# Kernel optimization log

Hardware: AMD Instinct MI355X
Metric: run time of the kernel (lower is better)

## Reference

```python
import jax, jax.numpy as jnp
import numpy as np

OWN_DIM = 7
INTR_DIM = 5
N_HEADS = 3
HEAD_DIM = 5
N_INTR = 256
ACT_DIM = 2
HID = 256
B = 16384


def setup_inputs() -> dict:
    key = jax.random.key(0)
    ks = jax.random.split(key, 16)
    def rn(k, shape, scale=0.1):
        return (jax.random.normal(k, shape, dtype=jnp.float32) * scale)
    obs = jax.random.normal(ks[0], (B, OWN_DIM + N_INTR * INTR_DIM), dtype=jnp.float32)
    in_dim = OWN_DIM + N_HEADS * HEAD_DIM  # 22
    return {
        "obs": obs,
        "Wq": rn(ks[1], (N_HEADS, HEAD_DIM, OWN_DIM)),
        "bq": rn(ks[2], (N_HEADS, HEAD_DIM)),
        "Wk": rn(ks[3], (N_HEADS, HEAD_DIM, INTR_DIM)),
        "bk": rn(ks[4], (N_HEADS, HEAD_DIM)),
        "Wv": rn(ks[5], (N_HEADS, HEAD_DIM, INTR_DIM)),
        "bv": rn(ks[6], (N_HEADS, HEAD_DIM)),
        "v_att": rn(ks[7], (N_HEADS, HEAD_DIM), 0.5),
        "temperature": jnp.ones((1,), dtype=jnp.float32) * 3.0,
        "W1": rn(ks[8], (in_dim, HID)),
        "b1": rn(ks[9], (HID,)),
        "W2": rn(ks[10], (HID, HID)),
        "b2": rn(ks[11], (HID,)),
        "Wf": rn(ks[12], (HID, ACT_DIM)),
        "bf": rn(ks[13], (ACT_DIM,)),
        "log_std": jnp.zeros((ACT_DIM,), dtype=jnp.float32),
    }


def reference(obs, Wq, bq, Wk, bk, Wv, bv, v_att, temperature,
              W1, b1, W2, b2, Wf, bf, log_std):
    own = obs[:, :OWN_DIM]                                   # [B,7]
    intr = obs[:, OWN_DIM:OWN_DIM + N_INTR * INTR_DIM].reshape(-1, N_INTR, INTR_DIM)  # [B,N,5]

    # per-head projections, all heads at once
    q = jnp.einsum('bo,hdo->bhd', own, Wq) + bq[None]        # [B,H,5]
    k = jnp.einsum('bni,hdi->bhnd', intr, Wk) + bk[None, :, None, :]  # [B,H,N,5]
    v = jnp.einsum('bni,hdi->bhnd', intr, Wv) + bv[None, :, None, :]  # [B,H,N,5]

    energy = jnp.tanh(q[:, :, None, :] + k)                  # [B,H,N,5]
    scores = jnp.einsum('bhnd,hd->bhn', energy, v_att)       # [B,H,N]
    scores = scores * jnp.abs(temperature)[0]

    is_padding = jnp.sum(jnp.abs(intr), axis=2) < 1e-6       # [B,N]
    scores = jnp.where(is_padding[:, None, :], -jnp.inf, scores)
    alpha = jax.nn.softmax(scores, axis=-1)                  # [B,H,N]
    alpha = jnp.nan_to_num(alpha, nan=0.0)

    context = jnp.einsum('bhn,bhnd->bhd', alpha, v).reshape(-1, N_HEADS * HEAD_DIM)  # [B,15]

    x = jnp.concatenate([own, context], axis=1)              # [B,22]
    x = jax.nn.leaky_relu(x @ W1 + b1, negative_slope=0.2)
    x = jax.nn.leaky_relu(x @ W2 + b2, negative_slope=0.2)
    out = x @ Wf + bf                                        # [B,2]
    log_std_exp = jnp.broadcast_to(log_std[None, :], (out.shape[0], ACT_DIM))
    return jnp.concatenate([out, log_std_exp], axis=1)       # [B,4]
```

## Files before the change

### kernel.cpp

```cpp
#include <hip/hip_runtime.h>
#include <math.h>

#define OWN_DIM 7
#define INTR_DIM 5
#define N_HEADS 3
#define HEAD_DIM 5
#define N_INTR 256
#define HID 256
#define BATCH 16384
#define ROW 1287

typedef __attribute__((ext_vector_type(8))) short bf16x8;
typedef __attribute__((ext_vector_type(4))) float f32x4;

__device__ __forceinline__ float fast_tanh(float x) {
    float e = __expf(2.0f * x);
    return 1.0f - 2.0f * __builtin_amdgcn_rcpf(e + 1.0f);
}

__device__ __forceinline__ float leaky(float x) {
    return x > 0.0f ? x : 0.2f * x;
}

__device__ __forceinline__ unsigned short f2bf(float f) {
    union { float f; unsigned u; } v; v.f = f;
    unsigned r = (v.u + 0x7FFFu + ((v.u >> 16) & 1u)) >> 16;
    return (unsigned short)r;
}

__device__ __forceinline__ unsigned pack2(unsigned short a, unsigned short b) {
    return (unsigned)a | ((unsigned)b << 16);
}

__global__ __launch_bounds__(256) void prep_kernel(
    const float* __restrict__ W1, const float* __restrict__ W2,
    unsigned short* __restrict__ W1t, unsigned short* __restrict__ W2t)
{
    int idx = blockIdx.x * 256 + threadIdx.x;
    int col = idx & 255;
    int kq = idx >> 8;
    ushort4 o;
    o.x = f2bf(W2[(kq * 4 + 0) * 256 + col]);
    o.y = f2bf(W2[(kq * 4 + 1) * 256 + col]);
    o.z = f2bf(W2[(kq * 4 + 2) * 256 + col]);
    o.w = f2bf(W2[(kq * 4 + 3) * 256 + col]);
    *((ushort4*)(W2t + col * 256 + kq * 4)) = o;
    if (kq < 8) {
        ushort4 p;
        int k = kq * 4;
        p.x = (k + 0) < 22 ? f2bf(W1[(k + 0) * 256 + col]) : 0;
        p.y = (k + 1) < 22 ? f2bf(W1[(k + 1) * 256 + col]) : 0;
        p.z = (k + 2) < 22 ? f2bf(W1[(k + 2) * 256 + col]) : 0;
        p.w = (k + 3) < 22 ? f2bf(W1[(k + 3) * 256 + col]) : 0;
        *((ushort4*)(W1t + col * 32 + k)) = p;
    }
}

__global__ __launch_bounds__(256, 4) void attn_kernel(
    const float* __restrict__ obs,
    const float* __restrict__ Wq, const float* __restrict__ bq,
    const float* __restrict__ Wk, const float* __restrict__ bk,
    const float* __restrict__ Wv, const float* __restrict__ bv,
    const float* __restrict__ v_att, const float* __restrict__ temperature,
    unsigned short* __restrict__ xb)
{
    __shared__ __align__(16) float srow[4 * ROW + 4];
    int tid = threadIdx.x;

    {
        const float4* src = (const float4*)(obs + (size_t)blockIdx.x * 4 * ROW);
        float4* dst = (float4*)srow;
        #pragma unroll
        for (int i = 0; i < 5; i++) dst[tid + 256 * i] = src[tid + 256 * i];
        if (tid < 1287 - 1280) dst[1280 + tid] = src[1280 + tid];
    }
    __syncthreads();

    int wave = tid >> 6;
    int lane = tid & 63;
    int b = blockIdx.x * 4 + wave;
    const float* row = srow + wave * ROW;

    float absT = fabsf(temperature[0]);

    float own[7];
    #pragma unroll
    for (int o = 0; o < 7; o++) own[o] = row[o];

    float q[15];
    #pragma unroll
    for (int hd = 0; hd < 15; hd++) {
        float acc = bq[hd];
        #pragma unroll
        for (int o = 0; o < 7; o++) acc = fmaf(own[o], Wq[hd * 7 + o], acc);
        q[hd] = acc;
    }
    float va[15];
    #pragma unroll
    for (int hd = 0; hd < 15; hd++) va[hd] = v_att[hd] * absT;

    float it[4][5];
    float sc[3][4];
    #pragma unroll
    for (int j = 0; j < 4; j++) {
        int n = lane + 64 * j;
        const float* ip = row + OWN_DIM + INTR_DIM * n;
        float asum = 0.0f;
        #pragma unroll
        for (int i = 0; i < 5; i++) { it[j][i] = ip[i]; asum += fabsf(it[j][i]); }
        bool pad = asum < 1e-6f;
        #pragma unroll
        for (int h = 0; h < 3; h++) {
            float s = 0.0f;
            #pragma unroll
            for (int d = 0; d < 5; d++) {
                float kd = bk[h * 5 + d];
                #pragma unroll
                for (int i = 0; i < 5; i++)
                    kd = fmaf(it[j][i], Wk[(h * 5 + d) * 5 + i], kd);
                float e = fast_tanh(q[h * 5 + d] + kd);
                s = fmaf(va[h * 5 + d], e, s);
            }
            sc[h][j] = pad ? -INFINITY : s;
        }
    }

    float alpha[3][4];
    float sa[3];
    #pragma unroll
    for (int h = 0; h < 3; h++) {
        float m = fmaxf(fmaxf(sc[h][0], sc[h][1]), fmaxf(sc[h][2], sc[h][3]));
        #pragma unroll
        for (int off = 32; off >= 1; off >>= 1) m = fmaxf(m, __shfl_xor(m, off));
        if (m < -3.0e38f) m = 0.0f;
        float lsum = 0.0f;
        #pragma unroll
        for (int j = 0; j < 4; j++) { alpha[h][j] = __expf(sc[h][j] - m); lsum += alpha[h][j]; }
        #pragma unroll
        for (int off = 32; off >= 1; off >>= 1) lsum += __shfl_xor(lsum, off);
        float rden = lsum > 0.0f ? __builtin_amdgcn_rcpf(lsum) : 0.0f;
        sa[h] = lsum > 0.0f ? 1.0f : 0.0f;
        #pragma unroll
        for (int j = 0; j < 4; j++) alpha[h][j] *= rden;
    }

    float ctx[15];
    #pragma unroll
    for (int hi = 0; hi < 15; hi++) ctx[hi] = 0.0f;
    #pragma unroll
    for (int h = 0; h < 3; h++)
        #pragma unroll
        for (int j = 0; j < 4; j++) {
            float a = alpha[h][j];
            #pragma unroll
            for (int i = 0; i < 5; i++)
                ctx[h * 5 + i] = fmaf(a, it[j][i], ctx[h * 5 + i]);
        }
    #pragma unroll
    for (int hi = 0; hi < 15; hi++) {
        float v = ctx[hi];
        #pragma unroll
        for (int off = 32; off >= 1; off >>= 1) v += __shfl_xor(v, off);
        ctx[hi] = v;
    }

    float x[22];
    #pragma unroll
    for (int o = 0; o < 7; o++) x[o] = own[o];
    #pragma unroll
    for (int hd = 0; hd < 15; hd++) {
        int h = hd / 5;
        float acc = bv[hd] * sa[h];
        #pragma unroll
        for (int i = 0; i < 5; i++)
            acc = fmaf(Wv[hd * 5 + i], ctx[h * 5 + i], acc);
        x[7 + hd] = acc;
    }

    unsigned short xs[24];
    #pragma unroll
    for (int i = 0; i < 22; i++) xs[i] = f2bf(x[i]);
    xs[22] = 0; xs[23] = 0;
    uint4 u0 = { pack2(xs[0], xs[1]),  pack2(xs[2], xs[3]),  pack2(xs[4], xs[5]),  pack2(xs[6], xs[7]) };
    uint4 u1 = { pack2(xs[8], xs[9]),  pack2(xs[10], xs[11]), pack2(xs[12], xs[13]), pack2(xs[14], xs[15]) };
    uint4 u2 = { pack2(xs[16], xs[17]), pack2(xs[18], xs[19]), pack2(xs[20], xs[21]), pack2(xs[22], xs[23]) };
    uint4 u3 = { 0u, 0u, 0u, 0u };
    uint4 lo = (lane & 1) ? u1 : u0;
    uint4 hi = (lane & 1) ? u3 : u2;
    uint4 sel = (lane & 2) ? hi : lo;
    if (lane < 4) {
        *((uint4*)(xb + (size_t)b * 32 + lane * 8)) = sel;
    }
}

__global__ __launch_bounds__(256, 2) void mlp_fused_kernel(
    const unsigned short* __restrict__ xb,
    const unsigned short* __restrict__ W1t, const unsigned short* __restrict__ W2t,
    const float* __restrict__ b1, const float* __restrict__ b2,
    const float* __restrict__ Wf, const float* __restrict__ bfv,
    const float* __restrict__ log_std, float* __restrict__ out)
{
    __shared__ unsigned short h1t[16 * 264];
    __shared__ float finbuf[2][4][16][2];

    int tid = threadIdx.x;
    int w = tid >> 6;
    int lane = tid & 63;
    int lm = lane & 15;
    int q = lane >> 4;
    int mbase = blockIdx.x * 32;

    float b1v[4], b2v[4], wf0[4], wf1[4];
    bf16x8 fw1[4];
    bf16x8 fw2[4][8];
    #pragma unroll
    for (int s = 0; s < 4; s++) {
        int col = w * 64 + s * 16 + lm;
        b1v[s] = b1[col];
        b2v[s] = b2[col];
        wf0[s] = Wf[col * 2];
        wf1[s] = Wf[col * 2 + 1];
        fw1[s] = *((const bf16x8*)(W1t + col * 32 + q * 8));
        #pragma unroll
        for (int t = 0; t < 8; t++)
            fw2[s][t] = *((const bf16x8*)(W2t + col * 256 + t * 32 + q * 8));
    }

    #pragma unroll
    for (int mt = 0; mt < 2; mt++) {
        int m0 = mbase + mt * 16;
        bf16x8 ax = *((const bf16x8*)(xb + (size_t)(m0 + lm) * 32 + q * 8));

        #pragma unroll
        for (int s = 0; s < 4; s++) {
            f32x4 c = {0.0f, 0.0f, 0.0f, 0.0f};
            c = __builtin_amdgcn_mfma_f32_16x16x32_bf16(ax, fw1[s], c, 0, 0, 0);
            int col = w * 64 + s * 16 + lm;
            #pragma unroll
            for (int i = 0; i < 4; i++)
                h1t[(q * 4 + i) * 264 + col] = f2bf(leaky(c[i] + b1v[s]));
        }
        __syncthreads();

        bf16x8 a2[8];
        #pragma unroll
        for (int t = 0; t < 8; t++)
            a2[t] = *((const bf16x8*)(h1t + lm * 264 + t * 32 + q * 8));

        float p0[4] = {0, 0, 0, 0};
        float p1[4] = {0, 0, 0, 0};
        #pragma unroll
        for (int s = 0; s < 4; s++) {
            f32x4 acc = {0.0f, 0.0f, 0.0f, 0.0f};
            #pragma unroll
            for (int t = 0; t < 8; t++)
                acc = __builtin_amdgcn_mfma_f32_16x16x32_bf16(a2[t], fw2[s][t], acc, 0, 0, 0);
            #pragma unroll
            for (int i = 0; i < 4; i++) {
                float h2 = leaky(acc[i] + b2v[s]);
                p0[i] = fmaf(h2, wf0[s], p0[i]);
                p1[i] = fmaf(h2, wf1[s], p1[i]);
            }
        }

        #pragma unroll
        for (int off = 1; off < 16; off <<= 1) {
            #pragma unroll
            for (int i = 0; i < 4; i++) {
                p0[i] += __shfl_xor(p0[i], off);
                p1[i] += __shfl_xor(p1[i], off);
            }
        }
        if (lm == 0) {
            #pragma unroll
            for (int i = 0; i < 4; i++) {
                finbuf[mt][w][q * 4 + i][0] = p0[i];
                finbuf[mt][w][q * 4 + i][1] = p1[i];
            }
        }
        __syncthreads();
        if (tid < 32) {
            int r = tid >> 1;
            int a = tid & 1;
            float s4 = finbuf[mt][0][r][a] + finbuf[mt][1][r][a]
                     + finbuf[mt][2][r][a] + finbuf[mt][3][r][a];
            out[(size_t)(m0 + r) * 4 + a] = s4 + bfv[a];
            out[(size_t)(m0 + r) * 4 + 2 + a] = log_std[a];
        }
    }
}

extern "C" void kernel_launch(void* const* d_in, const int* in_sizes, int n_in,
                              void* d_out, int out_size, void* d_ws, size_t ws_size,
                              hipStream_t stream) {
    const float* obs  = (const float*)d_in[0];
    const float* Wq   = (const float*)d_in[1];
    const float* bq   = (const float*)d_in[2];
    const float* Wk   = (const float*)d_in[3];
    const float* bk   = (const float*)d_in[4];
    const float* Wv   = (const float*)d_in[5];
    const float* bv   = (const float*)d_in[6];
    const float* v_att = (const float*)d_in[7];
    const float* temperature = (const float*)d_in[8];
    const float* W1   = (const float*)d_in[9];
    const float* b1   = (const float*)d_in[10];
    const float* W2   = (const float*)d_in[11];
    const float* b2   = (const float*)d_in[12];
    const float* Wf   = (const float*)d_in[13];
    const float* bf   = (const float*)d_in[14];
    const float* log_std = (const float*)d_in[15];
    float* out = (float*)d_out;

    unsigned short* xb  = (unsigned short*)d_ws;
    unsigned short* W1t = xb + (size_t)BATCH * 32;
    unsigned short* W2t = W1t + 256 * 32;

    prep_kernel<<<64, 256, 0, stream>>>(W1, W2, W1t, W2t);
    attn_kernel<<<BATCH / 4, 256, 0, stream>>>(
        obs, Wq, bq, Wk, bk, Wv, bv, v_att, temperature, xb);
    mlp_fused_kernel<<<BATCH / 32, 256, 0, stream>>>(
        xb, W1t, W2t, b1, b2, Wf, bf, log_std, out);
}
```

Before: 186.5 us.

## Fold tanh algebra into attention scores, merge weight prep into attention kernel

```diff
diff --git a/kernel.cpp b/kernel.cpp
--- a/kernel.cpp
+++ b/kernel.cpp
@@ -1,4 +1,5 @@
 #include <hip/hip_runtime.h>
+#include <hip/hip_bf16.h>
 #include <math.h>
 
 #define OWN_DIM 7
@@ -13,11 +14,6 @@
 typedef __attribute__((ext_vector_type(8))) short bf16x8;
 typedef __attribute__((ext_vector_type(4))) float f32x4;
 
-__device__ __forceinline__ float fast_tanh(float x) {
-    float e = __expf(2.0f * x);
-    return 1.0f - 2.0f * __builtin_amdgcn_rcpf(e + 1.0f);
-}
-
 __device__ __forceinline__ float leaky(float x) {
     return x > 0.0f ? x : 0.2f * x;
 }
@@ -28,32 +24,16 @@
     return (unsigned short)r;
 }
 
-__device__ __forceinline__ unsigned pack2(unsigned short a, unsigned short b) {
-    return (unsigned)a | ((unsigned)b << 16);
-}
-
-__global__ __launch_bounds__(256) void prep_kernel(
-    const float* __restrict__ W1, const float* __restrict__ W2,
-    unsigned short* __restrict__ W1t, unsigned short* __restrict__ W2t)
-{
-    int idx = blockIdx.x * 256 + threadIdx.x;
-    int col = idx & 255;
-    int kq = idx >> 8;
-    ushort4 o;
-    o.x = f2bf(W2[(kq * 4 + 0) * 256 + col]);
-    o.y = f2bf(W2[(kq * 4 + 1) * 256 + col]);
-    o.z = f2bf(W2[(kq * 4 + 2) * 256 + col]);
-    o.w = f2bf(W2[(kq * 4 + 3) * 256 + col]);
-    *((ushort4*)(W2t + col * 256 + kq * 4)) = o;
-    if (kq < 8) {
-        ushort4 p;
-        int k = kq * 4;
-        p.x = (k + 0) < 22 ? f2bf(W1[(k + 0) * 256 + col]) : 0;
-        p.y = (k + 1) < 22 ? f2bf(W1[(k + 1) * 256 + col]) : 0;
-        p.z = (k + 2) < 22 ? f2bf(W1[(k + 2) * 256 + col]) : 0;
-        p.w = (k + 3) < 22 ? f2bf(W1[(k + 3) * 256 + col]) : 0;
-        *((ushort4*)(W1t + col * 32 + k)) = p;
-    }
+__device__ __forceinline__ unsigned pkbf(float a, float b) {
+    __hip_bfloat162 h2 = __float22bfloat162_rn(make_float2(a, b));
+    unsigned u;
+    __builtin_memcpy(&u, &h2, 4);
+    return u;
+}
+
+__device__ __forceinline__ float rdlane(float v, int l) {
+    int iv = __builtin_bit_cast(int, v);
+    return __builtin_bit_cast(float, __builtin_amdgcn_readlane(iv, l));
 }
 
 __global__ __launch_bounds__(256, 4) void attn_kernel(
@@ -62,7 +42,9 @@
     const float* __restrict__ Wk, const float* __restrict__ bk,
     const float* __restrict__ Wv, const float* __restrict__ bv,
     const float* __restrict__ v_att, const float* __restrict__ temperature,
-    unsigned short* __restrict__ xb)
+    const float* __restrict__ W1, const float* __restrict__ W2,
+    unsigned short* __restrict__ xb,
+    unsigned short* __restrict__ W1t, unsigned short* __restrict__ W2t)
 {
     __shared__ __align__(16) float srow[4 * ROW + 4];
     int tid = threadIdx.x;
@@ -72,54 +54,74 @@
         float4* dst = (float4*)srow;
         #pragma unroll
         for (int i = 0; i < 5; i++) dst[tid + 256 * i] = src[tid + 256 * i];
-        if (tid < 1287 - 1280) dst[1280 + tid] = src[1280 + tid];
+        if (tid < 7) dst[1280 + tid] = src[1280 + tid];
+    }
+
+    int waveu = __builtin_amdgcn_readfirstlane(tid >> 6);
+    int lane = tid & 63;
+    int b = blockIdx.x * 4 + waveu;
+    const float* rowg = obs + (size_t)b * ROW;
+
+    float absT = fabsf(temperature[0]);
+    float own_s[7];
+    #pragma unroll
+    for (int o = 0; o < 7; o++) own_s[o] = rowg[o];
+
+    int hd = lane < 15 ? lane : 14;
+    float qv = bq[hd] + bk[hd];
+    #pragma unroll
+    for (int o = 0; o < 7; o++) qv = fmaf(own_s[o], Wq[hd * 7 + o], qv);
+    qv *= 2.0f;
+    float m2vav = -2.0f * absT * v_att[hd];
+
+    float qb2[15], m2va[15];
+    #pragma unroll
+    for (int i = 0; i < 15; i++) {
+        qb2[i] = rdlane(qv, i);
+        m2va[i] = rdlane(m2vav, i);
+    }
+    float Sva[3];
+    #pragma unroll
+    for (int h = 0; h < 3; h++) {
+        float s = 0.0f;
+        #pragma unroll
+        for (int d = 0; d < 5; d++) s += m2va[h * 5 + d];
+        Sva[h] = -0.5f * s;
     }
     __syncthreads();
 
-    int wave = tid >> 6;
-    int lane = tid & 63;
-    int b = blockIdx.x * 4 + wave;
-    const float* row = srow + wave * ROW;
-
-    float absT = fabsf(temperature[0]);
-
-    float own[7];
-    #pragma unroll
-    for (int o = 0; o < 7; o++) own[o] = row[o];
-
-    float q[15];
-    #pragma unroll
-    for (int hd = 0; hd < 15; hd++) {
-        float acc = bq[hd];
-        #pragma unroll
-        for (int o = 0; o < 7; o++) acc = fmaf(own[o], Wq[hd * 7 + o], acc);
-        q[hd] = acc;
-    }
-    float va[15];
-    #pragma unroll
-    for (int hd = 0; hd < 15; hd++) va[hd] = v_att[hd] * absT;
+    const float* row = srow + waveu * ROW;
 
     float it[4][5];
+    float asum[4];
+    #pragma unroll
+    for (int j = 0; j < 4; j++) {
+        const float* ip = row + OWN_DIM + INTR_DIM * (lane + 64 * j);
+        float a = 0.0f;
+        #pragma unroll
+        for (int i = 0; i < 5; i++) {
+            float v = ip[i];
+            it[j][i] = v + v;
+            a += fabsf(v);
+        }
+        asum[j] = a;
+    }
+
     float sc[3][4];
     #pragma unroll
     for (int j = 0; j < 4; j++) {
-        int n = lane + 64 * j;
-        const float* ip = row + OWN_DIM + INTR_DIM * n;
-        float asum = 0.0f;
-        #pragma unroll
-        for (int i = 0; i < 5; i++) { it[j][i] = ip[i]; asum += fabsf(it[j][i]); }
-        bool pad = asum < 1e-6f;
+        bool pad = asum[j] < 1e-6f;
         #pragma unroll
         for (int h = 0; h < 3; h++) {
-            float s = 0.0f;
+            float s = Sva[h];
             #pragma unroll
             for (int d = 0; d < 5; d++) {
-                float kd = bk[h * 5 + d];
+                float y = qb2[h * 5 + d];
                 #pragma unroll
                 for (int i = 0; i < 5; i++)
-                    kd = fmaf(it[j][i], Wk[(h * 5 + d) * 5 + i], kd);
-                float e = fast_tanh(q[h * 5 + d] + kd);
-                s = fmaf(va[h * 5 + d], e, s);
+                    y = fmaf(it[j][i], Wk[(h * 5 + d) * 5 + i], y);
+                float t = __expf(y) + 1.0f;
+                s = fmaf(m2va[h * 5 + d], __builtin_amdgcn_rcpf(t), s);
             }
             sc[h][j] = pad ? -INFINITY : s;
         }
@@ -138,15 +140,15 @@
         for (int j = 0; j < 4; j++) { alpha[h][j] = __expf(sc[h][j] - m); lsum += alpha[h][j]; }
         #pragma unroll
         for (int off = 32; off >= 1; off >>= 1) lsum += __shfl_xor(lsum, off);
-        float rden = lsum > 0.0f ? __builtin_amdgcn_rcpf(lsum) : 0.0f;
+        float rden = lsum > 0.0f ? 0.5f * __builtin_amdgcn_rcpf(lsum) : 0.0f;
         sa[h] = lsum > 0.0f ? 1.0f : 0.0f;
         #pragma unroll
         for (int j = 0; j < 4; j++) alpha[h][j] *= rden;
     }
 
-    float ctx[15];
-    #pragma unroll
-    for (int hi = 0; hi < 15; hi++) ctx[hi] = 0.0f;
+    float cp[15];
+    #pragma unroll
+    for (int i = 0; i < 15; i++) cp[i] = 0.0f;
     #pragma unroll
     for (int h = 0; h < 3; h++)
         #pragma unroll
@@ -154,42 +156,71 @@
             float a = alpha[h][j];
             #pragma unroll
             for (int i = 0; i < 5; i++)
-                ctx[h * 5 + i] = fmaf(a, it[j][i], ctx[h * 5 + i]);
-        }
-    #pragma unroll
-    for (int hi = 0; hi < 15; hi++) {
-        float v = ctx[hi];
-        #pragma unroll
-        for (int off = 32; off >= 1; off >>= 1) v += __shfl_xor(v, off);
-        ctx[hi] = v;
-    }
+                cp[h * 5 + i] = fmaf(a, it[j][i], cp[h * 5 + i]);
+        }
+    float* red = srow + waveu * ROW;
+    #pragma unroll
+    for (int i = 0; i < 15; i++) red[lane * 17 + i] = cp[i];
+    {
+        int q4 = lane >> 4, ci = lane & 15;
+        float ps = 0.0f;
+        #pragma unroll
+        for (int r = 0; r < 16; r++) ps += red[(q4 * 16 + r) * 17 + ci];
+        ps += __shfl_xor(ps, 16);
+        ps += __shfl_xor(ps, 32);
+        if (lane < 15) red[1090 + lane] = ps;
+    }
+    float ctx[15];
+    #pragma unroll
+    for (int i = 0; i < 15; i++) ctx[i] = red[1090 + i];
 
     float x[22];
     #pragma unroll
-    for (int o = 0; o < 7; o++) x[o] = own[o];
-    #pragma unroll
-    for (int hd = 0; hd < 15; hd++) {
-        int h = hd / 5;
-        float acc = bv[hd] * sa[h];
+    for (int o = 0; o < 7; o++) x[o] = own_s[o];
+    #pragma unroll
+    for (int k = 0; k < 15; k++) {
+        int h = k / 5;
+        float acc = bv[k] * sa[h];
         #pragma unroll
         for (int i = 0; i < 5; i++)
-            acc = fmaf(Wv[hd * 5 + i], ctx[h * 5 + i], acc);
-        x[7 + hd] = acc;
-    }
-
-    unsigned short xs[24];
-    #pragma unroll
-    for (int i = 0; i < 22; i++) xs[i] = f2bf(x[i]);
-    xs[22] = 0; xs[23] = 0;
-    uint4 u0 = { pack2(xs[0], xs[1]),  pack2(xs[2], xs[3]),  pack2(xs[4], xs[5]),  pack2(xs[6], xs[7]) };
-    uint4 u1 = { pack2(xs[8], xs[9]),  pack2(xs[10], xs[11]), pack2(xs[12], xs[13]), pack2(xs[14], xs[15]) };
-    uint4 u2 = { pack2(xs[16], xs[17]), pack2(xs[18], xs[19]), pack2(xs[20], xs[21]), pack2(xs[22], xs[23]) };
+            acc = fmaf(Wv[k * 5 + i], ctx[h * 5 + i], acc);
+        x[7 + k] = acc;
+    }
+
+    unsigned up[12];
+    #pragma unroll
+    for (int i = 0; i < 11; i++) up[i] = pkbf(x[2 * i], x[2 * i + 1]);
+    up[11] = 0u;
+    uint4 u0 = { up[0], up[1], up[2],  up[3] };
+    uint4 u1 = { up[4], up[5], up[6],  up[7] };
+    uint4 u2 = { up[8], up[9], up[10], up[11] };
     uint4 u3 = { 0u, 0u, 0u, 0u };
     uint4 lo = (lane & 1) ? u1 : u0;
     uint4 hi = (lane & 1) ? u3 : u2;
     uint4 sel = (lane & 2) ? hi : lo;
     if (lane < 4) {
         *((uint4*)(xb + (size_t)b * 32 + lane * 8)) = sel;
+    }
+
+    if (blockIdx.x < 64) {
+        int idx = blockIdx.x * 256 + tid;
+        int col = idx & 255;
+        int kq = idx >> 8;
+        ushort4 o;
+        o.x = f2bf(W2[(kq * 4 + 0) * 256 + col]);
+        o.y = f2bf(W2[(kq * 4 + 1) * 256 + col]);
+        o.z = f2bf(W2[(kq * 4 + 2) * 256 + col]);
+        o.w = f2bf(W2[(kq * 4 + 3) * 256 + col]);
+        *((ushort4*)(W2t + col * 256 + kq * 4)) = o;
+        if (kq < 8) {
+            ushort4 p;
+            int k = kq * 4;
+            p.x = (k + 0) < 22 ? f2bf(W1[(k + 0) * 256 + col]) : 0;
+            p.y = (k + 1) < 22 ? f2bf(W1[(k + 1) * 256 + col]) : 0;
+            p.z = (k + 2) < 22 ? f2bf(W1[(k + 2) * 256 + col]) : 0;
+            p.w = (k + 3) < 22 ? f2bf(W1[(k + 3) * 256 + col]) : 0;
+            *((ushort4*)(W1t + col * 32 + k)) = p;
+        }
     }
 }
 
@@ -315,9 +346,9 @@
     unsigned short* W1t = xb + (size_t)BATCH * 32;
     unsigned short* W2t = W1t + 256 * 32;
 
-    prep_kernel<<<64, 256, 0, stream>>>(W1, W2, W1t, W2t);
     attn_kernel<<<BATCH / 4, 256, 0, stream>>>(
-        obs, Wq, bq, Wk, bk, Wv, bv, v_att, temperature, xb);
+        obs, Wq, bq, Wk, bk, Wv, bv, v_att, temperature, W1, W2,
+        xb, W1t, W2t);
     mlp_fused_kernel<<<BATCH / 32, 256, 0, stream>>>(
         xb, W1t, W2t, b1, b2, Wf, bf, log_std, out);
 }
```

New measurement: 179.6 us. -3.7%, faster.
